# Performance work log

Measured on AMD Instinct MI355X. Metric: run time of the kernel, lower is better.

The kernel has to match this reference:

```python
import jax, jax.numpy as jnp
import numpy as np

B, D, N = 256, 128, 65536
P, K, P2 = 100, 4096, 10
T, MOM = 0.07, 0.5


def setup_inputs() -> dict:
    key = jax.random.key(0)
    k1, k2, k3, k4, k5 = jax.random.split(key, 5)
    stdv = 1.0 / np.sqrt(D / 3.0)
    memory_v1 = jax.random.uniform(k1, (N, D), minval=-stdv, maxval=stdv, dtype=jnp.float32)
    memory_v2 = jax.random.uniform(k2, (N, D), minval=-stdv, maxval=stdv, dtype=jnp.float32)
    v1 = jax.random.normal(k3, (B, D), dtype=jnp.float32)
    v2 = jax.random.normal(k4, (B, D), dtype=jnp.float32)
    y = jnp.arange(B, dtype=jnp.int32)  # unique sample ids in the bank
    idx = jax.random.randint(k5, (B, K + P), 0, N, dtype=jnp.int32)
    idx = idx.at[:, 0].set(y)  # first column is the ground-truth positive (as in torch)
    return {"epoch": 0, "v1": v1, "v2": v2, "y": y, "idx": idx,
            "memory_v1": memory_v1, "memory_v2": memory_v2}


def reference(epoch, v1, v2, y, idx, memory_v1, memory_v2):
    # --- gather contrastive keys from the memory banks (detached in torch) ---
    w1 = jax.lax.stop_gradient(memory_v1)[idx]  # [B, K+P, D]
    w2 = jax.lax.stop_gradient(memory_v2)[idx]  # [B, K+P, D]

    # similarity logits against the student feature v2
    out = jnp.exp(jnp.einsum('bkd,bd->bk', w1, v2) / T)  # [B, K+P]

    # --- hard positive selection via teacher/student relation gap ---
    t_rel = jnp.einsum('bkd,bd->bk',
                       w1 / jnp.linalg.norm(w1, axis=2, keepdims=True),
                       v1 / jnp.linalg.norm(v1, axis=1, keepdims=True))
    s_rel = jnp.einsum('bkd,bd->bk',
                       w2 / jnp.linalg.norm(w2, axis=2, keepdims=True),
                       v2 / jnp.linalg.norm(v2, axis=1, keepdims=True))
    diff = t_rel[:, :P] - s_rel[:, :P]            # [B, P]
    order = jnp.argsort(-diff, axis=1)            # descending sort ('hard' mode)
    sel = order[:, :P2].at[:, 0].set(0)           # force slot 0 = ground-truth positive

    out_pos = jnp.take_along_axis(out, sel, axis=1)  # [B, P2]
    out_neg = out[:, P:P + K]                        # [B, K]
    out_cat = jnp.concatenate([out_pos, out_neg], axis=1)  # [B, P2+K]

    # normalization constant Z (first-iteration estimate; a detached scalar in torch)
    Z = jax.lax.stop_gradient(out_cat.mean() * N)
    out_final = (out_cat / Z)[:, :, None]  # [B, P2+K, 1]

    # --- momentum memory update (no_grad in torch) ---
    l = memory_v1[y] * MOM + v1 * (1.0 - MOM)
    new_mem_v1 = memory_v1.at[y].set(l / jnp.linalg.norm(l, axis=1, keepdims=True))
    new_mem_v1 = jax.lax.stop_gradient(new_mem_v1)
    # (memory_v2 is updated identically in torch but not returned; omitted from outputs)

    return out_final, new_mem_v1
```

## Files before the change

kernel.cpp:

```cpp
#include <hip/hip_runtime.h>
#include <math.h>

constexpr int B_ = 256;
constexpr int D_ = 128;
constexpr int N_ = 65536;
constexpr int P_ = 100;
constexpr int K_ = 4096;
constexpr int P2_ = 10;
constexpr int KP_ = K_ + P_;
constexpr int OC_ = P2_ + K_;
constexpr int NBIN_ = 8;
constexpr int SLOT_ = 768;
constexpr int GCOS_ = B_;
constexpr int GCOPY_ = 2048;
constexpr int GGATH_ = B_ * NBIN_;
constexpr int NPART_ = GGATH_ + B_;
constexpr float T_ = 0.07f;

__global__ __launch_bounds__(256) void k_bin(
    const int* __restrict__ idx, unsigned* __restrict__ lists,
    int* __restrict__ counts)
{
  const int b = blockIdx.x;
  const int tid = threadIdx.x;
  __shared__ int cnt[NBIN_];
  if (tid < NBIN_) cnt[tid] = 0;
  __syncthreads();
  const int4* __restrict__ src = reinterpret_cast<const int4*>(idx + (size_t)b * KP_ + P_);
#pragma unroll
  for (int i = 0; i < 4; ++i) {
    const int4 r4 = src[i * 256 + tid];
    const int ks = (i * 256 + tid) * 4;
    const int rows[4] = {r4.x, r4.y, r4.z, r4.w};
#pragma unroll
    for (int u = 0; u < 4; ++u) {
      const int row = rows[u];
      const int bin = row >> 13;
      const int slot = atomicAdd(&cnt[bin], 1);
      if (slot < SLOT_)
        lists[((size_t)(b * NBIN_ + bin)) * SLOT_ + slot] =
            ((unsigned)(ks + u) << 16) | (unsigned)row;
    }
  }
  __syncthreads();
  if (tid < NBIN_) counts[b * NBIN_ + tid] = min(cnt[tid], SLOT_);
}

__global__ __launch_bounds__(256) void k_main(
    const float* __restrict__ v1, const float* __restrict__ v2,
    const int* __restrict__ idx, const float* __restrict__ mem1,
    const float* __restrict__ mem2, const unsigned* __restrict__ lists,
    const int* __restrict__ counts, float* __restrict__ evals,
    float* __restrict__ wsel, float* __restrict__ outmem,
    double* __restrict__ wpart)
{
  const int tid = threadIdx.x;
  const unsigned bid = blockIdx.x;
  __shared__ double lacc[4];
  __shared__ float sbuf[2 * D_];
  __shared__ double sdiff[P_];
  __shared__ float swout[P_];
  __shared__ double dsn2[P_], dss[P_];
  __shared__ double dinv[2];

  if (bid < GCOS_) {
    const int b = bid;
    if (tid < 32)
      reinterpret_cast<float4*>(sbuf)[tid] =
          reinterpret_cast<const float4*>(v2 + (size_t)b * D_)[tid];
    else if (tid < 64)
      reinterpret_cast<float4*>(sbuf)[tid] =
          reinterpret_cast<const float4*>(v1 + (size_t)b * D_)[tid - 32];
    __syncthreads();
    if (tid < 64) {
      const float2* s2 = reinterpret_cast<const float2*>(sbuf);
      const float2 a = s2[tid];
      const float2 c = s2[64 + tid];
      double dn2 = (double)a.x * a.x + (double)a.y * a.y;
      double dn1 = (double)c.x * c.x + (double)c.y * c.y;
#pragma unroll
      for (int sh = 1; sh < 64; sh <<= 1) {
        dn2 += __shfl_xor(dn2, sh);
        dn1 += __shfl_xor(dn1, sh);
      }
      if (tid == 0) { dinv[0] = 1.0 / sqrt(dn1); dinv[1] = 1.0 / sqrt(dn2); }
    }
    if (tid >= 128 && tid < 128 + P_) {
      const int r = tid - 128;
      const int row = idx[(size_t)b * KP_ + r];
      const float4* __restrict__ w2p = reinterpret_cast<const float4*>(mem2 + (size_t)row * D_);
      const float4* __restrict__ x2p = reinterpret_cast<const float4*>(sbuf);
      double sn2 = 0, ss = 0;
#pragma unroll 4
      for (int jj = 0; jj < 32; ++jj) {
        const float4 cc = w2p[jj];
        const float4 y2 = x2p[jj];
        sn2 += (double)cc.x * cc.x + (double)cc.y * cc.y + (double)cc.z * cc.z + (double)cc.w * cc.w;
        ss  += (double)cc.x * y2.x + (double)cc.y * y2.y + (double)cc.z * y2.z + (double)cc.w * y2.w;
      }
      dsn2[r] = sn2; dss[r] = ss;
    }
    double so = 0, sn1 = 0, st = 0;
    if (tid < P_) {
      const int row = idx[(size_t)b * KP_ + tid];
      const float4* __restrict__ w1p = reinterpret_cast<const float4*>(mem1 + (size_t)row * D_);
      const float4* __restrict__ x2p = reinterpret_cast<const float4*>(sbuf);
      const float4* __restrict__ x1p = reinterpret_cast<const float4*>(sbuf + D_);
#pragma unroll 4
      for (int jj = 0; jj < 32; ++jj) {
        const float4 a  = w1p[jj];
        const float4 y1 = x1p[jj];
        const float4 y2 = x2p[jj];
        so  += (double)a.x * y2.x + (double)a.y * y2.y + (double)a.z * y2.z + (double)a.w * y2.w;
        sn1 += (double)a.x * a.x  + (double)a.y * a.y  + (double)a.z * a.z  + (double)a.w * a.w;
        st  += (double)a.x * y1.x + (double)a.y * y1.y + (double)a.z * y1.z + (double)a.w * y1.w;
      }
    }
    __syncthreads();
    if (tid < P_) {
      const double t_rel = st * dinv[0] / sqrt(sn1);
      const double s_rel = dss[tid] * dinv[1] / sqrt(dsn2[tid]);
      sdiff[tid] = t_rel - s_rel;
      swout[tid] = expf((float)(so * (1.0 / (double)T_)));
    }
    __syncthreads();
    if (tid < 64) {
      const int l = tid;
      const double va = sdiff[l];
      const double vb = (l < P_ - 64) ? sdiff[l + 64] : -1.0e300;
      bool ta = false, tb = (l >= P_ - 64);
      int sel[P2_];
#pragma unroll
      for (int t = 0; t < P2_; ++t) {
        double cv; int cj;
        const bool aok = !ta, bok = !tb;
        if (aok && (!bok || va >= vb)) { cv = va; cj = l; }
        else if (bok)                  { cv = vb; cj = l + 64; }
        else                           { cv = -1.0e300; cj = 0x7fffffff; }
#pragma unroll
        for (int sh = 1; sh < 64; sh <<= 1) {
          const double ov = __shfl_xor(cv, sh);
          const int    oj = __shfl_xor(cj, sh);
          if (ov > cv || (ov == cv && oj < cj)) { cv = ov; cj = oj; }
        }
        sel[t] = cj;
        if (cj == l) ta = true;
        if (cj == l + 64) tb = true;
      }
      if (l == 0) {
        sel[0] = 0;
        double sp = 0.0;
#pragma unroll
        for (int t = 0; t < P2_; ++t) {
          const float e = swout[sel[t]];
          wsel[b * P2_ + t] = e;
          sp += (double)e;
        }
        wpart[GGATH_ + b] = sp;
      }
    }
  } else if (bid < GCOS_ + GCOPY_) {
    const int g = bid - GCOS_;
    const int r = g & 7, q = g >> 3;
    const size_t base = ((size_t)r * 8192 + (size_t)q * 32) * D_;
    const float4* __restrict__ s = reinterpret_cast<const float4*>(mem1 + base);
    float4* __restrict__ d = reinterpret_cast<float4*>(outmem + base);
#pragma unroll
    for (int i = 0; i < 4; ++i) d[i * 256 + tid] = s[i * 256 + tid];
  } else {
    const int g = bid - GCOS_ - GCOPY_;
    const int bin = g & 7, b = g >> 3;
    const int count = counts[b * NBIN_ + bin];
    const unsigned* __restrict__ lb = lists + ((size_t)(b * NBIN_ + bin)) * SLOT_;
    float* __restrict__ eb = evals + ((size_t)(b * NBIN_ + bin)) * SLOT_;
    const int j = tid & 7, gg = tid >> 3;
    const float4* __restrict__ v2p = reinterpret_cast<const float4*>(v2 + (size_t)b * D_);
    const float4 x0 = v2p[j], x1 = v2p[j + 8], x2 = v2p[j + 16], x3 = v2p[j + 24];

    double de = 0.0;
    int s = gg;
    for (; s + 96 < count; s += 128) {
      const unsigned e0 = lb[s];
      const unsigned e1 = lb[s + 32];
      const unsigned e2 = lb[s + 64];
      const unsigned e3 = lb[s + 96];
      const float4* __restrict__ p0 = reinterpret_cast<const float4*>(mem1 + (size_t)(e0 & 0xFFFFu) * D_);
      const float4* __restrict__ p1 = reinterpret_cast<const float4*>(mem1 + (size_t)(e1 & 0xFFFFu) * D_);
      const float4* __restrict__ p2 = reinterpret_cast<const float4*>(mem1 + (size_t)(e2 & 0xFFFFu) * D_);
      const float4* __restrict__ p3 = reinterpret_cast<const float4*>(mem1 + (size_t)(e3 & 0xFFFFu) * D_);
      const float4 a0 = p0[j], a1 = p0[j + 8], a2 = p0[j + 16], a3 = p0[j + 24];
      const float4 b0 = p1[j], b1 = p1[j + 8], b2 = p1[j + 16], b3 = p1[j + 24];
      const float4 c0 = p2[j], c1 = p2[j + 8], c2 = p2[j + 16], c3 = p2[j + 24];
      const float4 d0 = p3[j], d1 = p3[j + 8], d2 = p3[j + 16], d3 = p3[j + 24];
      float s0 = a0.x * x0.x + a0.y * x0.y + a0.z * x0.z + a0.w * x0.w
               + a1.x * x1.x + a1.y * x1.y + a1.z * x1.z + a1.w * x1.w
               + a2.x * x2.x + a2.y * x2.y + a2.z * x2.z + a2.w * x2.w
               + a3.x * x3.x + a3.y * x3.y + a3.z * x3.z + a3.w * x3.w;
      float s1 = b0.x * x0.x + b0.y * x0.y + b0.z * x0.z + b0.w * x0.w
               + b1.x * x1.x + b1.y * x1.y + b1.z * x1.z + b1.w * x1.w
               + b2.x * x2.x + b2.y * x2.y + b2.z * x2.z + b2.w * x2.w
               + b3.x * x3.x + b3.y * x3.y + b3.z * x3.z + b3.w * x3.w;
      float s2v = c0.x * x0.x + c0.y * x0.y + c0.z * x0.z + c0.w * x0.w
                + c1.x * x1.x + c1.y * x1.y + c1.z * x1.z + c1.w * x1.w
                + c2.x * x2.x + c2.y * x2.y + c2.z * x2.z + c2.w * x2.w
                + c3.x * x3.x + c3.y * x3.y + c3.z * x3.z + c3.w * x3.w;
      float s3v = d0.x * x0.x + d0.y * x0.y + d0.z * x0.z + d0.w * x0.w
                + d1.x * x1.x + d1.y * x1.y + d1.z * x1.z + d1.w * x1.w
                + d2.x * x2.x + d2.y * x2.y + d2.z * x2.z + d2.w * x2.w
                + d3.x * x3.x + d3.y * x3.y + d3.z * x3.z + d3.w * x3.w;
#pragma unroll
      for (int sh = 1; sh < 8; sh <<= 1) {
        s0 += __shfl_xor(s0, sh);
        s1 += __shfl_xor(s1, sh);
        s2v += __shfl_xor(s2v, sh);
        s3v += __shfl_xor(s3v, sh);
      }
      if (j == 0) {
        const float f0 = expf(s0 * (1.0f / T_));
        const float f1 = expf(s1 * (1.0f / T_));
        const float f2 = expf(s2v * (1.0f / T_));
        const float f3 = expf(s3v * (1.0f / T_));
        eb[s] = f0; eb[s + 32] = f1; eb[s + 64] = f2; eb[s + 96] = f3;
        de += ((double)f0 + (double)f1) + ((double)f2 + (double)f3);
      }
    }
    for (; s < count; s += 32) {
      const unsigned e0 = lb[s];
      const float4* __restrict__ p0 = reinterpret_cast<const float4*>(mem1 + (size_t)(e0 & 0xFFFFu) * D_);
      const float4 a0 = p0[j], a1 = p0[j + 8], a2 = p0[j + 16], a3 = p0[j + 24];
      float s0 = a0.x * x0.x + a0.y * x0.y + a0.z * x0.z + a0.w * x0.w
               + a1.x * x1.x + a1.y * x1.y + a1.z * x1.z + a1.w * x1.w
               + a2.x * x2.x + a2.y * x2.y + a2.z * x2.z + a2.w * x2.w
               + a3.x * x3.x + a3.y * x3.y + a3.z * x3.z + a3.w * x3.w;
#pragma unroll
      for (int sh = 1; sh < 8; sh <<= 1) s0 += __shfl_xor(s0, sh);
      if (j == 0) {
        const float f0 = expf(s0 * (1.0f / T_));
        eb[s] = f0;
        de += (double)f0;
      }
    }
#pragma unroll
    for (int sh = 1; sh < 64; sh <<= 1) de += __shfl_xor(de, sh);
    if ((tid & 63) == 0) lacc[tid >> 6] = de;
    __syncthreads();
    if (tid == 0) wpart[g] = (lacc[0] + lacc[1]) + (lacc[2] + lacc[3]);
  }
}

__global__ __launch_bounds__(256) void k_z(
    const double* __restrict__ wpart, float* __restrict__ invz)
{
  __shared__ double lds[4];
  const int tid = threadIdx.x;
  double s = 0.0;
  for (int i = tid; i < NPART_; i += 256) s += wpart[i];
#pragma unroll
  for (int sh = 1; sh < 64; sh <<= 1) s += __shfl_xor(s, sh);
  if ((tid & 63) == 0) lds[tid >> 6] = s;
  __syncthreads();
  if (tid == 0) {
    const double S = (lds[0] + lds[1]) + (lds[2] + lds[3]);
    const double Z = S / ((double)B_ * (double)OC_) * (double)N_;
    *invz = (float)(1.0 / Z);
  }
}

__global__ __launch_bounds__(256) void k_out(
    const unsigned* __restrict__ lists, const int* __restrict__ counts,
    const float* __restrict__ evals, const float* __restrict__ wsel,
    const float* __restrict__ invz, const float* __restrict__ mem1,
    const float* __restrict__ v1, const int* __restrict__ y,
    float* __restrict__ out, float* __restrict__ outmem)
{
  __shared__ float srow[K_];
  const int b = blockIdx.x;
  const int tid = threadIdx.x;
  const float sc = *invz;
#pragma unroll
  for (int bin = 0; bin < NBIN_; ++bin) {
    const int cnt = counts[b * NBIN_ + bin];
    const unsigned* __restrict__ lb = lists + ((size_t)(b * NBIN_ + bin)) * SLOT_;
    const float* __restrict__ eb = evals + ((size_t)(b * NBIN_ + bin)) * SLOT_;
    for (int s = tid; s < cnt; s += 256) srow[lb[s] >> 16] = eb[s];
  }
  __syncthreads();
  float* __restrict__ orow = out + (size_t)b * OC_;
  if (tid < P2_) orow[tid] = wsel[b * P2_ + tid] * sc;
  for (int i = tid; i < K_; i += 256) orow[P2_ + i] = srow[i] * sc;
  if (tid < 64) {
    const int row = y[b];
    const float2 m = *reinterpret_cast<const float2*>(mem1 + (size_t)row * D_ + tid * 2);
    const float2 a = *reinterpret_cast<const float2*>(v1 + (size_t)b * D_ + tid * 2);
    float2 l;
    l.x = m.x * 0.5f + a.x * 0.5f;
    l.y = m.y * 0.5f + a.y * 0.5f;
    float n = l.x * l.x + l.y * l.y;
#pragma unroll
    for (int sh = 1; sh < 64; sh <<= 1) n += __shfl_xor(n, sh);
    const float inv = 1.0f / sqrtf(n);
    float2 o;
    o.x = l.x * inv;
    o.y = l.y * inv;
    *reinterpret_cast<float2*>(outmem + (size_t)row * D_ + tid * 2) = o;
  }
}

extern "C" void kernel_launch(void* const* d_in, const int* in_sizes, int n_in,
                              void* d_out, int out_size, void* d_ws, size_t ws_size,
                              hipStream_t stream) {
  const float* v1   = (const float*)d_in[1];
  const float* v2   = (const float*)d_in[2];
  const int*   y    = (const int*)d_in[3];
  const int*   idx  = (const int*)d_in[4];
  const float* mem1 = (const float*)d_in[5];
  const float* mem2 = (const float*)d_in[6];

  float* out    = (float*)d_out;
  float* outmem = out + (size_t)B_ * OC_;

  char* ws = (char*)d_ws;
  constexpr size_t LSZ = (size_t)B_ * NBIN_ * SLOT_ * 4;
  double*   wpart  = (double*)ws;
  int*      counts = (int*)(ws + 32768);
  unsigned* lists  = (unsigned*)(ws + 65536);
  float*    evals  = (float*)(ws + 65536 + LSZ);
  float*    wsel   = (float*)(ws + 65536 + 2 * LSZ);
  float*    invz   = (float*)(ws + 65536 + 2 * LSZ + 16384);

  k_bin<<<B_, 256, 0, stream>>>(idx, lists, counts);
  k_main<<<GCOS_ + GCOPY_ + GGATH_, 256, 0, stream>>>(
      v1, v2, idx, mem1, mem2, lists, counts, evals, wsel, outmem, wpart);
  k_z<<<1, 256, 0, stream>>>(wpart, invz);
  k_out<<<B_, 256, 0, stream>>>(lists, counts, evals, wsel, invz,
                                mem1, v1, y, out, outmem);
}
```

Before: 65.99 us.

## Use 16 row bins and 16-lane dot products with 8-way gather unroll

Doubles the number of memory-bank row bins (each covering 4096 rows with 384 slots), so twice as many gather blocks each handle smaller lists. The copy blocks are remapped to match the new bin ranges. Each row dot product now uses 16 lanes with two float4 loads instead of 8 lanes with four, and each lane issues 8 independent row loads per iteration to raise memory-level parallelism. The trade-off is more blocks and partials, clamped redundant loads at list tails, and a higher overflow risk with 384 slots per bin (expected about 256 entries each).

```diff
diff --git a/kernel.cpp b/kernel.cpp
--- a/kernel.cpp
+++ b/kernel.cpp
@@ -9,9 +9,9 @@
 constexpr int P2_ = 10;
 constexpr int KP_ = K_ + P_;
 constexpr int OC_ = P2_ + K_;
-constexpr int NBIN_ = 8;
-constexpr int SLOT_ = 768;
-constexpr int GCOS_ = B_;
+constexpr int NBIN_ = 16;
+constexpr int SLOT_ = 384;
+constexpr int GCOS_ = 256;
 constexpr int GCOPY_ = 2048;
 constexpr int GGATH_ = B_ * NBIN_;
 constexpr int NPART_ = GGATH_ + B_;
@@ -35,7 +35,7 @@
 #pragma unroll
     for (int u = 0; u < 4; ++u) {
       const int row = rows[u];
-      const int bin = row >> 13;
+      const int bin = row >> 12;
       const int slot = atomicAdd(&cnt[bin], 1);
       if (slot < SLOT_)
         lists[((size_t)(b * NBIN_ + bin)) * SLOT_ + slot] =
@@ -162,82 +162,50 @@
   } else if (bid < GCOS_ + GCOPY_) {
     const int g = bid - GCOS_;
     const int r = g & 7, q = g >> 3;
-    const size_t base = ((size_t)r * 8192 + (size_t)q * 32) * D_;
+    const size_t row0 = (q < 128) ? ((size_t)r * 4096 + (size_t)q * 32)
+                                  : ((size_t)(r + 8) * 4096 + (size_t)(q - 128) * 32);
+    const size_t base = row0 * D_;
     const float4* __restrict__ s = reinterpret_cast<const float4*>(mem1 + base);
     float4* __restrict__ d = reinterpret_cast<float4*>(outmem + base);
 #pragma unroll
     for (int i = 0; i < 4; ++i) d[i * 256 + tid] = s[i * 256 + tid];
   } else {
     const int g = bid - GCOS_ - GCOPY_;
-    const int bin = g & 7, b = g >> 3;
+    const int bin = g & 15, b = g >> 4;
     const int count = counts[b * NBIN_ + bin];
     const unsigned* __restrict__ lb = lists + ((size_t)(b * NBIN_ + bin)) * SLOT_;
     float* __restrict__ eb = evals + ((size_t)(b * NBIN_ + bin)) * SLOT_;
-    const int j = tid & 7, gg = tid >> 3;
+    const int j = tid & 15, gg = tid >> 4;
     const float4* __restrict__ v2p = reinterpret_cast<const float4*>(v2 + (size_t)b * D_);
-    const float4 x0 = v2p[j], x1 = v2p[j + 8], x2 = v2p[j + 16], x3 = v2p[j + 24];
+    const float4 x0 = v2p[j], x1 = v2p[j + 16];
 
     double de = 0.0;
-    int s = gg;
-    for (; s + 96 < count; s += 128) {
-      const unsigned e0 = lb[s];
-      const unsigned e1 = lb[s + 32];
-      const unsigned e2 = lb[s + 64];
-      const unsigned e3 = lb[s + 96];
-      const float4* __restrict__ p0 = reinterpret_cast<const float4*>(mem1 + (size_t)(e0 & 0xFFFFu) * D_);
-      const float4* __restrict__ p1 = reinterpret_cast<const float4*>(mem1 + (size_t)(e1 & 0xFFFFu) * D_);
-      const float4* __restrict__ p2 = reinterpret_cast<const float4*>(mem1 + (size_t)(e2 & 0xFFFFu) * D_);
-      const float4* __restrict__ p3 = reinterpret_cast<const float4*>(mem1 + (size_t)(e3 & 0xFFFFu) * D_);
-      const float4 a0 = p0[j], a1 = p0[j + 8], a2 = p0[j + 16], a3 = p0[j + 24];
-      const float4 b0 = p1[j], b1 = p1[j + 8], b2 = p1[j + 16], b3 = p1[j + 24];
-      const float4 c0 = p2[j], c1 = p2[j + 8], c2 = p2[j + 16], c3 = p2[j + 24];
-      const float4 d0 = p3[j], d1 = p3[j + 8], d2 = p3[j + 16], d3 = p3[j + 24];
-      float s0 = a0.x * x0.x + a0.y * x0.y + a0.z * x0.z + a0.w * x0.w
-               + a1.x * x1.x + a1.y * x1.y + a1.z * x1.z + a1.w * x1.w
-               + a2.x * x2.x + a2.y * x2.y + a2.z * x2.z + a2.w * x2.w
-               + a3.x * x3.x + a3.y * x3.y + a3.z * x3.z + a3.w * x3.w;
-      float s1 = b0.x * x0.x + b0.y * x0.y + b0.z * x0.z + b0.w * x0.w
-               + b1.x * x1.x + b1.y * x1.y + b1.z * x1.z + b1.w * x1.w
-               + b2.x * x2.x + b2.y * x2.y + b2.z * x2.z + b2.w * x2.w
-               + b3.x * x3.x + b3.y * x3.y + b3.z * x3.z + b3.w * x3.w;
-      float s2v = c0.x * x0.x + c0.y * x0.y + c0.z * x0.z + c0.w * x0.w
-                + c1.x * x1.x + c1.y * x1.y + c1.z * x1.z + c1.w * x1.w
-                + c2.x * x2.x + c2.y * x2.y + c2.z * x2.z + c2.w * x2.w
-                + c3.x * x3.x + c3.y * x3.y + c3.z * x3.z + c3.w * x3.w;
-      float s3v = d0.x * x0.x + d0.y * x0.y + d0.z * x0.z + d0.w * x0.w
-                + d1.x * x1.x + d1.y * x1.y + d1.z * x1.z + d1.w * x1.w
-                + d2.x * x2.x + d2.y * x2.y + d2.z * x2.z + d2.w * x2.w
-                + d3.x * x3.x + d3.y * x3.y + d3.z * x3.z + d3.w * x3.w;
-#pragma unroll
-      for (int sh = 1; sh < 8; sh <<= 1) {
-        s0 += __shfl_xor(s0, sh);
-        s1 += __shfl_xor(s1, sh);
-        s2v += __shfl_xor(s2v, sh);
-        s3v += __shfl_xor(s3v, sh);
-      }
-      if (j == 0) {
-        const float f0 = expf(s0 * (1.0f / T_));
-        const float f1 = expf(s1 * (1.0f / T_));
-        const float f2 = expf(s2v * (1.0f / T_));
-        const float f3 = expf(s3v * (1.0f / T_));
-        eb[s] = f0; eb[s + 32] = f1; eb[s + 64] = f2; eb[s + 96] = f3;
-        de += ((double)f0 + (double)f1) + ((double)f2 + (double)f3);
-      }
-    }
-    for (; s < count; s += 32) {
-      const unsigned e0 = lb[s];
-      const float4* __restrict__ p0 = reinterpret_cast<const float4*>(mem1 + (size_t)(e0 & 0xFFFFu) * D_);
-      const float4 a0 = p0[j], a1 = p0[j + 8], a2 = p0[j + 16], a3 = p0[j + 24];
-      float s0 = a0.x * x0.x + a0.y * x0.y + a0.z * x0.z + a0.w * x0.w
-               + a1.x * x1.x + a1.y * x1.y + a1.z * x1.z + a1.w * x1.w
-               + a2.x * x2.x + a2.y * x2.y + a2.z * x2.z + a2.w * x2.w
-               + a3.x * x3.x + a3.y * x3.y + a3.z * x3.z + a3.w * x3.w;
-#pragma unroll
-      for (int sh = 1; sh < 8; sh <<= 1) s0 += __shfl_xor(s0, sh);
-      if (j == 0) {
-        const float f0 = expf(s0 * (1.0f / T_));
-        eb[s] = f0;
-        de += (double)f0;
+    for (int s = gg; s < count; s += 128) {
+      unsigned en[8];
+#pragma unroll
+      for (int u = 0; u < 8; ++u) {
+        const int p = s + u * 16;
+        en[u] = lb[p < SLOT_ ? p : SLOT_ - 1];
+      }
+      float4 ra[8], rb[8];
+#pragma unroll
+      for (int u = 0; u < 8; ++u) {
+        const float4* __restrict__ rp =
+            reinterpret_cast<const float4*>(mem1 + (size_t)(en[u] & 0xFFFFu) * D_);
+        ra[u] = rp[j];
+        rb[u] = rp[j + 16];
+      }
+#pragma unroll
+      for (int u = 0; u < 8; ++u) {
+        float d = ra[u].x * x0.x + ra[u].y * x0.y + ra[u].z * x0.z + ra[u].w * x0.w
+                + rb[u].x * x1.x + rb[u].y * x1.y + rb[u].z * x1.z + rb[u].w * x1.w;
+#pragma unroll
+        for (int sh = 1; sh < 16; sh <<= 1) d += __shfl_xor(d, sh);
+        if (j == 0 && s + u * 16 < count) {
+          const float f = expf(d * (1.0f / T_));
+          eb[s + u * 16] = f;
+          de += (double)f;
+        }
       }
     }
 #pragma unroll
@@ -322,7 +290,7 @@
   char* ws = (char*)d_ws;
   constexpr size_t LSZ = (size_t)B_ * NBIN_ * SLOT_ * 4;
   double*   wpart  = (double*)ws;
-  int*      counts = (int*)(ws + 32768);
+  int*      counts = (int*)(ws + 40960);
   unsigned* lists  = (unsigned*)(ws + 65536);
   float*    evals  = (float*)(ws + 65536 + LSZ);
   float*    wsel   = (float*)(ws + 65536 + 2 * LSZ);
```

After: 80.21 us. 1.22x slower.
